# Optimization experiments

Measured on AMD Instinct MI355X. Metric: run time of the kernel, lower is better.

The kernel has to match this reference:

```python
import jax, jax.numpy as jnp
import numpy as np

D = 256            # voxel grid resolution per axis
B, H, N = 1, 480 * 640, 9   # batch, pixels, samples per ray


def setup_inputs() -> dict:
    key = jax.random.key(0)
    k1, k2, k3 = jax.random.split(key, 3)
    # ray sample points in voxel coordinates; range slightly exceeds the grid
    # so the out-of-bounds masking path is exercised.
    points = jax.random.uniform(k1, (B, H, N, 3), dtype=jnp.float32,
                                minval=-2.0, maxval=float(D) + 1.0)
    tsdf_volume = jax.random.normal(k2, (D, D, D), dtype=jnp.float32)
    weights_volume = jax.random.uniform(k3, (D, D, D), dtype=jnp.float32)
    return {"points": points, "tsdf_volume": tsdf_volume,
            "weights_volume": weights_volume}


# binary corner offsets in the same (i, j, k) loop order as the original
_OFFS = np.array([[(c >> 2) & 1, (c >> 1) & 1, c & 1] for c in range(8)],
                 dtype=np.float32)  # [8, 3]


def _trilinear(points, tsdf_volume, weights_volume):
    b, h, n, _ = points.shape
    p = points.reshape(-1, 3)                      # [M, 3]
    idx = jnp.floor(p)
    center = idx + 0.5                             # mode='center'
    neighbor = jnp.sign(center - p)                # +-1 (0 exactly at center)
    alpha = jnp.abs(p - center)                    # [M, 3]
    alpha_inv = 1.0 - alpha
    offs = jnp.asarray(_OFFS, dtype=p.dtype)       # [8, 3]
    # per-corner trilinear weight: prod over dims of (alpha_inv if off==0 else alpha)
    w = jnp.prod(jnp.where(offs[None] == 0,
                           alpha_inv[:, None, :], alpha[:, None, :]),
                 axis=-1)                          # [M, 8]
    corner = idx[:, None, :] + offs[None] * neighbor[:, None, :]  # [M, 8, 3]
    ci = corner.astype(jnp.int32)
    dims = jnp.asarray(tsdf_volume.shape, dtype=jnp.int32)
    valid = jnp.all((ci >= 0) & (ci < dims[None, None, :]), axis=-1)  # [M, 8]
    cc = jnp.clip(ci, 0, dims[None, None, :] - 1)
    vmask = valid.astype(p.dtype)
    tv = tsdf_volume[cc[..., 0], cc[..., 1], cc[..., 2]] * vmask      # [M, 8]
    wv = weights_volume[cc[..., 0], cc[..., 1], cc[..., 2]] * vmask   # [M, 8]
    fusion_values = jnp.sum(tv * w, axis=1).reshape(b, h, n)
    fusion_weights = jnp.sum(wv * w, axis=1).reshape(b, h, n)
    indices = ci.reshape(b, h, n, 8, 3)
    weights = w.reshape(b, h, n, 8)
    return fusion_values, indices, weights, fusion_weights


def reference(points, tsdf_volume, weights_volume):
    return _trilinear(points, tsdf_volume, weights_volume)
```

## Files before the change

### kernel.cpp

```cpp
#include <hip/hip_runtime.h>


typedef float v2f __attribute__((ext_vector_type(2)));
typedef float v4f __attribute__((ext_vector_type(4)));

__global__ __launch_bounds__(256) void pack_kernel(
    const float* __restrict__ tsdf,
    const float* __restrict__ wvol,
    float* __restrict__ packed,
    int n4)
{
    const int i = blockIdx.x * 256 + threadIdx.x;
    if (i >= n4) return;
    const v4f t = *reinterpret_cast<const v4f*>(tsdf + 4ull * (size_t)i);
    const v4f w = *reinterpret_cast<const v4f*>(wvol + 4ull * (size_t)i);
    v4f a; a.x = t.x; a.y = w.x; a.z = t.y; a.w = w.y;
    v4f b; b.x = t.z; b.y = w.z; b.z = t.w; b.w = w.w;
    v4f* __restrict__ dst = reinterpret_cast<v4f*>(packed + 8ull * (size_t)i);
    dst[0] = a;
    dst[1] = b;
}

__global__ __launch_bounds__(256) void extractor_packed(
    const float* __restrict__ points,
    const float* __restrict__ packed,
    float* __restrict__ out,
    int M)
{
    const int m = blockIdx.x * 256 + threadIdx.x;
    if (m >= M) return;

    const size_t p3 = 3ull * (size_t)m;
    const float px = points[p3 + 0];
    const float py = points[p3 + 1];
    const float pz = points[p3 + 2];

    const float fx = floorf(px), fy = floorf(py), fz = floorf(pz);
    const int bx = (int)fx, by = (int)fy, bz = (int)fz;

    const float dxc = fx + 0.5f - px;
    const float dyc = fy + 0.5f - py;
    const float dzc = fz + 0.5f - pz;

    const int nx = (dxc > 0.f) ? 1 : ((dxc < 0.f) ? -1 : 0);
    const int ny = (dyc > 0.f) ? 1 : ((dyc < 0.f) ? -1 : 0);
    const int nz = (dzc > 0.f) ? 1 : ((dzc < 0.f) ? -1 : 0);

    const float ax = fabsf(dxc), ay = fabsf(dyc), az = fabsf(dzc);
    const float axi = 1.f - ax, ayi = 1.f - ay, azi = 1.f - az;

    float fv = 0.f, fw = 0.f;
    float idxf[24];
    float wts[8];

#pragma unroll
    for (int c = 0; c < 8; ++c) {
        const int ox = (c >> 2) & 1;
        const int oy = (c >> 1) & 1;
        const int oz = c & 1;
        const int cx = bx + (ox ? nx : 0);
        const int cy = by + (oy ? ny : 0);
        const int cz = bz + (oz ? nz : 0);
        const float w = (ox ? ax : axi) * (oy ? ay : ayi) * (oz ? az : azi);
        const bool valid = ((unsigned)cx < 256u) & ((unsigned)cy < 256u) & ((unsigned)cz < 256u);
        const int ccx = min(max(cx, 0), 255);
        const int ccy = min(max(cy, 0), 255);
        const int ccz = min(max(cz, 0), 255);
        const int flat = (ccx << 16) | (ccy << 8) | ccz;
        const float vm = valid ? 1.f : 0.f;
        const v2f tw = *reinterpret_cast<const v2f*>(packed + 2ull * (size_t)flat);
        fv += tw.x * vm * w;
        fw += tw.y * vm * w;
        idxf[c * 3 + 0] = (float)cx;
        idxf[c * 3 + 1] = (float)cy;
        idxf[c * 3 + 2] = (float)cz;
        wts[c] = w;
    }

    const size_t Ms = (size_t)M;
    out[m] = fv;
    out[33 * Ms + m] = fw;

    float4* __restrict__ oi = reinterpret_cast<float4*>(out + Ms + (size_t)m * 24);
    const float4* ii = reinterpret_cast<const float4*>(idxf);
#pragma unroll
    for (int i = 0; i < 6; ++i) oi[i] = ii[i];

    float4* __restrict__ ow = reinterpret_cast<float4*>(out + 25 * Ms + (size_t)m * 8);
    const float4* wi = reinterpret_cast<const float4*>(wts);
    ow[0] = wi[0];
    ow[1] = wi[1];
}

__global__ __launch_bounds__(256) void extractor_kernel(
    const float* __restrict__ points,
    const float* __restrict__ tsdf,
    const float* __restrict__ wvol,
    float* __restrict__ out,
    int M)
{
    const int m = blockIdx.x * 256 + threadIdx.x;
    if (m >= M) return;

    const size_t p3 = 3ull * (size_t)m;
    const float px = points[p3 + 0];
    const float py = points[p3 + 1];
    const float pz = points[p3 + 2];

    const float fx = floorf(px), fy = floorf(py), fz = floorf(pz);
    const int bx = (int)fx, by = (int)fy, bz = (int)fz;

    const float dxc = fx + 0.5f - px;
    const float dyc = fy + 0.5f - py;
    const float dzc = fz + 0.5f - pz;

    const int nx = (dxc > 0.f) ? 1 : ((dxc < 0.f) ? -1 : 0);
    const int ny = (dyc > 0.f) ? 1 : ((dyc < 0.f) ? -1 : 0);
    const int nz = (dzc > 0.f) ? 1 : ((dzc < 0.f) ? -1 : 0);

    const float ax = fabsf(dxc), ay = fabsf(dyc), az = fabsf(dzc);
    const float axi = 1.f - ax, ayi = 1.f - ay, azi = 1.f - az;

    float fv = 0.f, fw = 0.f;
    float idxf[24];
    float wts[8];

#pragma unroll
    for (int c = 0; c < 8; ++c) {
        const int ox = (c >> 2) & 1;
        const int oy = (c >> 1) & 1;
        const int oz = c & 1;
        const int cx = bx + (ox ? nx : 0);
        const int cy = by + (oy ? ny : 0);
        const int cz = bz + (oz ? nz : 0);
        const float w = (ox ? ax : axi) * (oy ? ay : ayi) * (oz ? az : azi);
        const bool valid = ((unsigned)cx < 256u) & ((unsigned)cy < 256u) & ((unsigned)cz < 256u);
        const int ccx = min(max(cx, 0), 255);
        const int ccy = min(max(cy, 0), 255);
        const int ccz = min(max(cz, 0), 255);
        const int flat = (ccx << 16) | (ccy << 8) | ccz;
        const float vm = valid ? 1.f : 0.f;
        const float tv = tsdf[flat] * vm;
        const float wv = wvol[flat] * vm;
        fv += tv * w;
        fw += wv * w;
        idxf[c * 3 + 0] = (float)cx;
        idxf[c * 3 + 1] = (float)cy;
        idxf[c * 3 + 2] = (float)cz;
        wts[c] = w;
    }

    const size_t Ms = (size_t)M;
    out[m] = fv;
    out[33 * Ms + m] = fw;

    float4* __restrict__ oi = reinterpret_cast<float4*>(out + Ms + (size_t)m * 24);
    const float4* ii = reinterpret_cast<const float4*>(idxf);
#pragma unroll
    for (int i = 0; i < 6; ++i) oi[i] = ii[i];

    float4* __restrict__ ow = reinterpret_cast<float4*>(out + 25 * Ms + (size_t)m * 8);
    const float4* wi = reinterpret_cast<const float4*>(wts);
    ow[0] = wi[0];
    ow[1] = wi[1];
}

extern "C" void kernel_launch(void* const* d_in, const int* in_sizes, int n_in,
                              void* d_out, int out_size, void* d_ws, size_t ws_size,
                              hipStream_t stream) {
    const float* points = (const float*)d_in[0];
    const float* tsdf   = (const float*)d_in[1];
    const float* wvol   = (const float*)d_in[2];
    float* out = (float*)d_out;

    const int M = in_sizes[0] / 3;
    const int blocks = (M + 255) / 256;

    const size_t nvox = 256ull * 256ull * 256ull;
    const size_t needed = nvox * 2ull * sizeof(float);

    if (ws_size >= needed) {
        float* packed = (float*)d_ws;
        const int n4 = (int)(nvox / 4);
        pack_kernel<<<(n4 + 255) / 256, 256, 0, stream>>>(tsdf, wvol, packed, n4);
        extractor_packed<<<blocks, 256, 0, stream>>>(points, packed, out, M);
    } else {
        extractor_kernel<<<blocks, 256, 0, stream>>>(points, tsdf, wvol, out, M);
    }
}
```

Before: 712.3 us.

## Pack TSDF and weight volumes into 2x2x2 bricks for gather locality

Replaces the linear interleaved packing of the tsdf and weight volumes with a 2x2x2 brick layout, so each brick's eight (tsdf, weight) pairs occupy 64 contiguous bytes. The extractor computes brick and in-brick offsets instead of a flat index. The aim is for each point's eight corner fetches to touch fewer cache lines than the four separate x/y rows of the linear layout. The pack kernel now does strided 8-byte reads, and corner windows that straddle brick boundaries still touch several bricks.

```diff
diff --git a/kernel.cpp b/kernel.cpp
--- a/kernel.cpp
+++ b/kernel.cpp
@@ -4,21 +4,35 @@
 typedef float v2f __attribute__((ext_vector_type(2)));
 typedef float v4f __attribute__((ext_vector_type(4)));
 
-__global__ __launch_bounds__(256) void pack_kernel(
+__global__ __launch_bounds__(256) void pack_brick_kernel(
     const float* __restrict__ tsdf,
     const float* __restrict__ wvol,
-    float* __restrict__ packed,
-    int n4)
+    float* __restrict__ packed)
 {
-    const int i = blockIdx.x * 256 + threadIdx.x;
-    if (i >= n4) return;
-    const v4f t = *reinterpret_cast<const v4f*>(tsdf + 4ull * (size_t)i);
-    const v4f w = *reinterpret_cast<const v4f*>(wvol + 4ull * (size_t)i);
-    v4f a; a.x = t.x; a.y = w.x; a.z = t.y; a.w = w.y;
-    v4f b; b.x = t.z; b.y = w.z; b.z = t.w; b.w = w.w;
-    v4f* __restrict__ dst = reinterpret_cast<v4f*>(packed + 8ull * (size_t)i);
-    dst[0] = a;
-    dst[1] = b;
+    const int t = blockIdx.x * 256 + threadIdx.x;
+    const int bz = t & 127;
+    const int by = (t >> 7) & 127;
+    const int bx = t >> 14;
+    const int x0 = bx << 1, y0 = by << 1, z0 = bz << 1;
+
+    v4f o[4];
+#pragma unroll
+    for (int dx = 0; dx < 2; ++dx) {
+#pragma unroll
+        for (int dy = 0; dy < 2; ++dy) {
+            const size_t src = ((size_t)(x0 + dx) << 16) |
+                               (size_t)((y0 + dy) << 8) | (size_t)z0;
+            const v2f tp = *reinterpret_cast<const v2f*>(tsdf + src);
+            const v2f wp = *reinterpret_cast<const v2f*>(wvol + src);
+            v4f o4; o4.x = tp.x; o4.y = wp.x; o4.z = tp.y; o4.w = wp.y;
+            o[dx * 2 + dy] = o4;
+        }
+    }
+    v4f* __restrict__ dst = reinterpret_cast<v4f*>(packed + ((size_t)t << 4));
+    dst[0] = o[0];
+    dst[1] = o[1];
+    dst[2] = o[2];
+    dst[3] = o[3];
 }
 
 __global__ __launch_bounds__(256) void extractor_packed(
@@ -66,9 +80,11 @@
         const int ccx = min(max(cx, 0), 255);
         const int ccy = min(max(cy, 0), 255);
         const int ccz = min(max(cz, 0), 255);
-        const int flat = (ccx << 16) | (ccy << 8) | ccz;
+        const int brick = ((ccx >> 1) << 14) | ((ccy >> 1) << 7) | (ccz >> 1);
+        const int off = ((ccx & 1) << 2) | ((ccy & 1) << 1) | (ccz & 1);
+        const size_t fidx = ((size_t)brick << 4) + (size_t)(off << 1);
         const float vm = valid ? 1.f : 0.f;
-        const v2f tw = *reinterpret_cast<const v2f*>(packed + 2ull * (size_t)flat);
+        const v2f tw = *reinterpret_cast<const v2f*>(packed + fidx);
         fv += tw.x * vm * w;
         fw += tw.y * vm * w;
         idxf[c * 3 + 0] = (float)cx;
@@ -181,8 +197,8 @@
 
     if (ws_size >= needed) {
         float* packed = (float*)d_ws;
-        const int n4 = (int)(nvox / 4);
-        pack_kernel<<<(n4 + 255) / 256, 256, 0, stream>>>(tsdf, wvol, packed, n4);
+        const int nbricks = 128 * 128 * 128;
+        pack_brick_kernel<<<nbricks / 256, 256, 0, stream>>>(tsdf, wvol, packed);
         extractor_packed<<<blocks, 256, 0, stream>>>(points, packed, out, M);
     } else {
         extractor_kernel<<<blocks, 256, 0, stream>>>(points, tsdf, wvol, out, M);
```

After: 705.1 us. Within noise of the previous version (-1.0%).
